# Kernel tuning notes

Measured on AMD Instinct MI355X. Metric: run time of the kernel, lower is better.

Reference implementation:

```python
import jax, jax.numpy as jnp
import numpy as np

K_UPPER = 196608  # number of smallest-|grad| positions to mask per sample


def setup_inputs() -> dict:
    key = jax.random.key(0)
    k1, k2 = jax.random.split(key)
    x = jax.random.normal(k1, (64, 3, 512, 512), dtype=jnp.float32)
    grad = jax.random.normal(k2, (64, 3, 512, 512), dtype=jnp.float32)
    return {"x": x, "grad": grad}


def _mask_low_gradient(x, grad):
    # x, grad: [B, C, H, W]
    B, C, H, W = x.shape
    hw = H * W
    flat_g = grad.reshape(B, -1)                                  # [B, C*H*W]
    # _sort: k smallest absolute gradients -> top_k of negated abs (unsorted ok)
    _neg_vals, idx = jax.lax.top_k(-jnp.abs(flat_g), K_UPPER)     # idx: [B, K]
    # channel containing each selected flat index (matches the torch range test)
    ch = idx // hw                                                # [B, K]
    xc = x.reshape(B, C, hw)
    # Faithful to source: torch slice [start:channel_indexes] EXCLUDES the last
    # element of each channel when computing min/max.
    mn = jnp.min(xc[:, :, : hw - 1], axis=-1)                     # [B, C]
    mx = jnp.max(xc[:, :, : hw - 1], axis=-1)                     # [B, C]
    lo = jnp.take_along_axis(mn, ch, axis=1)                      # [B, K]
    hi = jnp.take_along_axis(mx, ch, axis=1)                      # [B, K]
    # uniform fill in [lo, hi) per masked element
    u = jax.random.uniform(jax.random.key(42), idx.shape, dtype=x.dtype)
    fill = lo + u * (hi - lo)                                     # [B, K]
    flat_x = x.reshape(B, -1)
    out = flat_x.at[jnp.arange(B)[:, None], idx].set(fill)
    return out.reshape(x.shape)


def reference(x, grad):
    return _mask_low_gradient(x, grad)
```

## Files before the change

kernel.cpp:

```cpp
#include <hip/hip_runtime.h>
#include <stdint.h>

#define TPB 256
#define TPS 1024

constexpr int BN   = 64;
constexpr int CCH  = 3;
constexpr int HWS  = 262144;
constexpr int LOG_HW = 18;
constexpr int NPS  = 786432;
constexpr int KSEL = 196608;
constexpr int KCAP = 200704;
constexpr int NB_T = 32;
constexpr int CH_T = NPS / NB_T;
constexpr int NB_C = 64;
constexpr int CH_C = NPS / NB_C;
constexpr int WCH  = CH_C / 4;
constexpr int NB_S = 8;
constexpr int CH_S = KCAP / NB_S;
constexpr int TILE = 4096;
constexpr int NBINS = 2048;
constexpr int SUB  = 8;

constexpr int WS_MN   = 0;
constexpr int WS_MX   = 192;
constexpr int WS_V1   = 384;
constexpr int WS_B1   = 448;
constexpr int WS_GS   = 512;
constexpr int WS_KP   = 576;
constexpr int WS_S0   = 640;
constexpr int WS_S01  = 704;
constexpr int WS_CNT  = 768;
constexpr int WS_COFF = WS_CNT + BN * 256;
constexpr int WS_MNP  = WS_COFF + BN * 256;
constexpr int WS_MXP  = WS_MNP + BN * CCH * SUB;
constexpr int WS_CHC  = WS_MXP + BN * CCH * SUB;
constexpr int WS_THA  = WS_CHC + BN * 4;
constexpr int WS_THB  = WS_THA + BN * NBINS;
constexpr int WS_H0   = WS_THB + BN * NBINS;
constexpr int WS_H1   = WS_H0 + BN * 256 * NB_S;
constexpr int WS_H2   = WS_H1 + BN * 256 * NB_S;
constexpr int WS_H3   = WS_H2 + BN * 256 * NB_S;
constexpr size_t WS_FIX_END = (size_t)WS_H3 + (size_t)BN * 256 * NB_S;
constexpr size_t RECW = (size_t)BN * KCAP * 2;
constexpr size_t WS_NEEDED_BYTES = (WS_FIX_END + 2 * RECW) * 4;

__device__ __forceinline__ unsigned rotl32(unsigned x, int r) { return (x << r) | (x >> (32 - r)); }

__device__ __forceinline__ void tf4(unsigned& x0, unsigned& x1, int a, int b, int c, int d) {
  x0 += x1; x1 = rotl32(x1, a); x1 ^= x0;
  x0 += x1; x1 = rotl32(x1, b); x1 ^= x0;
  x0 += x1; x1 = rotl32(x1, c); x1 ^= x0;
  x0 += x1; x1 = rotl32(x1, d); x1 ^= x0;
}

__device__ __forceinline__ void threefry2x32(unsigned k0, unsigned k1, unsigned c0, unsigned c1,
                                             unsigned& o0, unsigned& o1) {
  const unsigned ks2 = k0 ^ k1 ^ 0x1BD11BDAu;
  unsigned x0 = c0 + k0, x1 = c1 + k1;
  tf4(x0, x1, 13, 15, 26, 6);  x0 += k1;  x1 += ks2 + 1u;
  tf4(x0, x1, 17, 29, 16, 24); x0 += ks2; x1 += k0 + 2u;
  tf4(x0, x1, 13, 15, 26, 6);  x0 += k0;  x1 += k1 + 3u;
  tf4(x0, x1, 17, 29, 16, 24); x0 += k1;  x1 += ks2 + 4u;
  tf4(x0, x1, 13, 15, 26, 6);  x0 += ks2; x1 += k0 + 5u;
  o0 = x0; o1 = x1;
}

__global__ __launch_bounds__(TPB) void k_zero(unsigned* __restrict__ p, int n) {
  int i = blockIdx.x * TPB + threadIdx.x;
  if (i < n) p[i] = 0u;
}

__global__ __launch_bounds__(TPB) void k_mnmx(const float4* __restrict__ x,
                                              unsigned* __restrict__ ws) {
  __shared__ float smn[TPB], smx[TPB];
  const int g = blockIdx.x;
  const int bc = g / SUB, sub = g - bc * SUB;
  const int Q4 = HWS / 4 / SUB;
  const size_t base4 = (size_t)bc * (HWS / 4) + (size_t)sub * Q4;
  const bool last = (sub == SUB - 1);
  const int tid = threadIdx.x;
  float lo = 3.4e38f, hi = -3.4e38f;
  for (int i = tid; i < Q4; i += TPB) {
    float4 v = x[base4 + i];
    if (last && i == Q4 - 1) {
      lo = fminf(lo, fminf(fminf(v.x, v.y), v.z));
      hi = fmaxf(hi, fmaxf(fmaxf(v.x, v.y), v.z));
    } else {
      lo = fminf(lo, fminf(fminf(v.x, v.y), fminf(v.z, v.w)));
      hi = fmaxf(hi, fmaxf(fmaxf(v.x, v.y), fmaxf(v.z, v.w)));
    }
  }
  smn[tid] = lo; smx[tid] = hi; __syncthreads();
  for (int s = TPB / 2; s > 0; s >>= 1) {
    if (tid < s) { smn[tid] = fminf(smn[tid], smn[tid + s]); smx[tid] = fmaxf(smx[tid], smx[tid + s]); }
    __syncthreads();
  }
  if (tid == 0) {
    ((float*)(ws + WS_MNP))[g] = smn[0];
    ((float*)(ws + WS_MXP))[g] = smx[0];
  }
}

__global__ __launch_bounds__(TPB) void k_mnfin(unsigned* __restrict__ ws) {
  const int t = threadIdx.x;
  if (t < BN * CCH) {
    const float* mnp = (const float*)(ws + WS_MNP);
    const float* mxp = (const float*)(ws + WS_MXP);
    float lo = 3.4e38f, hi = -3.4e38f;
    for (int s = 0; s < SUB; ++s) {
      lo = fminf(lo, mnp[t * SUB + s]);
      hi = fmaxf(hi, mxp[t * SUB + s]);
    }
    ((float*)(ws + WS_MN))[t] = lo;
    ((float*)(ws + WS_MX))[t] = hi;
  }
}

__global__ __launch_bounds__(TPB) void k_thrA(const unsigned* __restrict__ gb, unsigned* __restrict__ hist) {
  __shared__ unsigned h[NBINS];
  const int b = blockIdx.y, blk = blockIdx.x, tid = threadIdx.x;
  for (int v = tid; v < NBINS; v += TPB) h[v] = 0u;
  __syncthreads();
  const uint4* g4 = (const uint4*)(gb + (size_t)b * NPS + (size_t)blk * CH_T);
  for (int i = tid; i < CH_T / 4; i += TPB) {
    uint4 v = g4[i];
    atomicAdd(&h[(v.x & 0x7FFFFFFFu) >> 21], 1u);
    atomicAdd(&h[(v.y & 0x7FFFFFFFu) >> 21], 1u);
    atomicAdd(&h[(v.z & 0x7FFFFFFFu) >> 21], 1u);
    atomicAdd(&h[(v.w & 0x7FFFFFFFu) >> 21], 1u);
  }
  __syncthreads();
  unsigned* gh = hist + (size_t)b * NBINS;
  for (int v = tid; v < NBINS; v += TPB) if (h[v]) atomicAdd(&gh[v], h[v]);
}

__global__ __launch_bounds__(TPB) void k_thrB(const unsigned* __restrict__ gb,
                                              unsigned* __restrict__ hist,
                                              const unsigned* __restrict__ ws) {
  __shared__ unsigned h[NBINS];
  const int b = blockIdx.y, blk = blockIdx.x, tid = threadIdx.x;
  for (int v = tid; v < NBINS; v += TPB) h[v] = 0u;
  __syncthreads();
  const unsigned sel = ws[WS_V1 + b];
  const uint4* g4 = (const uint4*)(gb + (size_t)b * NPS + (size_t)blk * CH_T);
  for (int i = tid; i < CH_T / 4; i += TPB) {
    uint4 v = g4[i];
    unsigned a0 = v.x & 0x7FFFFFFFu, a1 = v.y & 0x7FFFFFFFu;
    unsigned a2 = v.z & 0x7FFFFFFFu, a3 = v.w & 0x7FFFFFFFu;
    if ((a0 >> 21) == sel) atomicAdd(&h[(a0 >> 10) & 2047u], 1u);
    if ((a1 >> 21) == sel) atomicAdd(&h[(a1 >> 10) & 2047u], 1u);
    if ((a2 >> 21) == sel) atomicAdd(&h[(a2 >> 10) & 2047u], 1u);
    if ((a3 >> 21) == sel) atomicAdd(&h[(a3 >> 10) & 2047u], 1u);
  }
  __syncthreads();
  unsigned* gh = hist + (size_t)b * NBINS;
  for (int v = tid; v < NBINS; v += TPB) if (h[v]) atomicAdd(&gh[v], h[v]);
}

__global__ __launch_bounds__(TPB) void k_find(const unsigned* __restrict__ hist,
                                              unsigned* __restrict__ ws, int mode) {
  __shared__ unsigned part[TPB];
  const int b = blockIdx.x, tid = threadIdx.x;
  const unsigned* h = hist + (size_t)b * NBINS;
  const int per = NBINS / TPB;
  const unsigned Kt = (mode == 0) ? (unsigned)KSEL : (unsigned)KSEL - ws[WS_B1 + b];
  unsigned vals[8];
  unsigned s = 0;
  for (int j = 0; j < per; ++j) { vals[j] = h[tid * per + j]; s += vals[j]; }
  part[tid] = s; __syncthreads();
  for (int off = 1; off < TPB; off <<= 1) {
    unsigned t = (tid >= off) ? part[tid - off] : 0u;
    __syncthreads(); part[tid] += t; __syncthreads();
  }
  unsigned run = part[tid] - s;
  for (int j = 0; j < per; ++j) {
    const unsigned lo = run, c = vals[j];
    run += c;
    if (lo < Kt && Kt <= run) {
      const unsigned v = (unsigned)(tid * per + j);
      if (mode == 0) {
        ws[WS_V1 + b] = v; ws[WS_B1 + b] = lo;
      } else {
        const unsigned T22 = (ws[WS_V1 + b] << 11) | v;
        ws[WS_GS + b] = (T22 << 10) | 1023u;
        unsigned kp = ws[WS_B1 + b] + lo + c;
        if (kp > (unsigned)KCAP) kp = (unsigned)KCAP;
        ws[WS_KP + b] = kp;
      }
    }
  }
}

__global__ __launch_bounds__(TPB) void k_ccount(const unsigned* __restrict__ gb, unsigned* __restrict__ ws) {
  __shared__ unsigned chs[3];
  const int b = blockIdx.y, blk = blockIdx.x, tid = threadIdx.x;
  const int lane = tid & 63, wv = tid >> 6;
  if (tid < 3) chs[tid] = 0u;
  __syncthreads();
  const unsigned G = ws[WS_GS + b];
  const uint4* g4 = (const uint4*)(gb + (size_t)b * NPS + (size_t)blk * CH_C) + wv * (WCH / 4);
  const unsigned e0 = (unsigned)blk * CH_C + (unsigned)wv * WCH;
  unsigned cnt = 0, cc0 = 0, cc1 = 0, cc2 = 0;
  for (int it = 0; it < WCH / 256; ++it) {
    const uint4 v = g4[it * 64 + lane];
    const unsigned e = e0 + (unsigned)it * 256u + (unsigned)lane * 4u;
    const unsigned k[4] = { v.x & 0x7FFFFFFFu, v.y & 0x7FFFFFFFu, v.z & 0x7FFFFFFFu, v.w & 0x7FFFFFFFu };
#pragma unroll
    for (int c = 0; c < 4; ++c) {
      if (k[c] <= G) {
        ++cnt;
        const unsigned ch = (e + (unsigned)c) >> LOG_HW;
        if (ch == 0) ++cc0; else if (ch == 1) ++cc1; else ++cc2;
      }
    }
  }
  for (int off = 32; off >= 1; off >>= 1) cnt += __shfl_down(cnt, off, 64);
  if (lane == 0) ws[WS_CNT + b * 256 + blk * 4 + wv] = cnt;
  if (cc0) atomicAdd(&chs[0], cc0);
  if (cc1) atomicAdd(&chs[1], cc1);
  if (cc2) atomicAdd(&chs[2], cc2);
  __syncthreads();
  if (tid < 3 && chs[tid]) atomicAdd(&ws[WS_CHC + b * 4 + tid], chs[tid]);
}

__global__ __launch_bounds__(TPB) void k_cscan(unsigned* __restrict__ ws) {
  __shared__ unsigned wsum[4];
  const int b = blockIdx.x, tid = threadIdx.x;
  const int lane = tid & 63, wv = tid >> 6;
  const unsigned cnt = ws[WS_CNT + b * 256 + tid];
  unsigned incl = cnt;
  for (int off = 1; off < 64; off <<= 1) {
    unsigned t = __shfl_up(incl, off, 64);
    if (lane >= off) incl += t;
  }
  if (lane == 63) wsum[wv] = incl;
  __syncthreads();
  unsigned wpre = 0;
  for (int w = 0; w < wv; ++w) wpre += wsum[w];
  ws[WS_COFF + b * 256 + tid] = incl - cnt + wpre;
  if (tid == 0) {
    const unsigned s0 = ws[WS_CHC + b * 4 + 0];
    ws[WS_S0 + b] = s0;
    ws[WS_S01 + b] = s0 + ws[WS_CHC + b * 4 + 1];
  }
}

__global__ __launch_bounds__(TPB) void k_cscatter(const unsigned* __restrict__ gb,
                                                  const unsigned* __restrict__ ws,
                                                  unsigned* __restrict__ keyArr,
                                                  unsigned* __restrict__ H0) {
  __shared__ unsigned h2[256 * NB_S];
  const int b = blockIdx.y, blk = blockIdx.x, tid = threadIdx.x;
  const int lane = tid & 63, wv = tid >> 6;
  for (int e = tid; e < 256 * NB_S; e += TPB) h2[e] = 0u;
  __syncthreads();
  const unsigned G = ws[WS_GS + b];
  unsigned base = ws[WS_COFF + b * 256 + blk * 4 + wv];
  const uint4* g4 = (const uint4*)(gb + (size_t)b * NPS + (size_t)blk * CH_C) + wv * (WCH / 4);
  unsigned* ka = keyArr + (size_t)b * KCAP;
  for (int it = 0; it < WCH / 256; ++it) {
    const uint4 v = g4[it * 64 + lane];
    unsigned k[4] = { v.x & 0x7FFFFFFFu, v.y & 0x7FFFFFFFu, v.z & 0x7FFFFFFFu, v.w & 0x7FFFFFFFu };
    bool s[4];
    unsigned cnt = 0;
#pragma unroll
    for (int c = 0; c < 4; ++c) { s[c] = (k[c] <= G); cnt += (unsigned)s[c]; }
    unsigned incl = cnt;
    for (int off = 1; off < 64; off <<= 1) {
      unsigned u = __shfl_up(incl, off, 64);
      if (lane >= off) incl += u;
    }
    const unsigned wtot = __shfl(incl, 63, 64);
    unsigned pos = base + incl - cnt;
#pragma unroll
    for (int c = 0; c < 4; ++c) {
      if (s[c]) {
        if (pos < (unsigned)KCAP) {
          ka[pos] = k[c];
          atomicAdd(&h2[(k[c] & 255u) * NB_S + pos / (unsigned)CH_S], 1u);
        }
        ++pos;
      }
    }
    base += wtot;
  }
  __syncthreads();
  unsigned* Hb = H0 + (size_t)b * 256 * NB_S;
  for (int e = tid; e < 256 * NB_S; e += TPB) {
    unsigned c = h2[e];
    if (c) atomicAdd(&Hb[e], c);
  }
}

__global__ __launch_bounds__(TPB) void k_hscan(unsigned* __restrict__ H) {
  __shared__ unsigned wsum[4];
  const int b = blockIdx.x, tid = threadIdx.x;
  const int lane = tid & 63, wv = tid >> 6;
  unsigned* Hb = H + (size_t)b * 256 * NB_S;
  unsigned row[NB_S];
  unsigned run = 0;
#pragma unroll
  for (int k = 0; k < NB_S; ++k) {
    unsigned t = Hb[tid * NB_S + k];
    row[k] = run; run += t;
  }
  unsigned incl = run;
  for (int off = 1; off < 64; off <<= 1) {
    unsigned t = __shfl_up(incl, off, 64);
    if (lane >= off) incl += t;
  }
  if (lane == 63) wsum[wv] = incl;
  __syncthreads();
  unsigned wpre = 0;
  for (int w = 0; w < wv; ++w) wpre += wsum[w];
  const unsigned excl = incl - run + wpre;
#pragma unroll
  for (int k = 0; k < NB_S; ++k) Hb[tid * NB_S + k] = row[k] + excl;
}

template<int MODE>
__global__ __launch_bounds__(TPS) void k_sort8(const unsigned* __restrict__ keyIn,
                                               const uint2* __restrict__ inR,
                                               uint2* __restrict__ outR,
                                               unsigned* __restrict__ fillmap,
                                               const unsigned* __restrict__ Hcur,
                                               unsigned* __restrict__ Hnext,
                                               const unsigned* __restrict__ ws,
                                               int shift) {
  __shared__ unsigned wh[16][256];
  __shared__ unsigned gout[256];
  __shared__ unsigned gbase[256];
  __shared__ unsigned wsum[4];
  __shared__ uint2    stg[(MODE == 2) ? 1 : TILE];
  __shared__ unsigned h2[(MODE == 2) ? 1 : 256 * NB_S];
  const int b = blockIdx.y, blk = blockIdx.x, tid = threadIdx.x;
  const int lane = tid & 63, wv = tid >> 6;
  const unsigned long long ltm = (1ull << lane) - 1ull;
  const unsigned kp = min(ws[WS_KP + b], (unsigned)KCAP);
  const unsigned s0 = (unsigned)blk * CH_S;
  const unsigned s1 = min(s0 + (unsigned)CH_S, kp);
  const unsigned* ki = keyIn + (size_t)b * KCAP;
  const uint2* in = inR + (size_t)b * KCAP;
  uint2* out = outR + (size_t)b * KCAP;
  unsigned* fm = fillmap + (size_t)b * KCAP;

  unsigned S0 = 0, S01 = 0;
  float l0 = 0, l1 = 0, l2 = 0, h0 = 0, h1 = 0, h2v = 0;
  if (MODE == 2) {
    S0 = ws[WS_S0 + b]; S01 = ws[WS_S01 + b];
    const float* mnf = (const float*)(ws + WS_MN);
    const float* mxf = (const float*)(ws + WS_MX);
    l0 = mnf[b * CCH]; l1 = mnf[b * CCH + 1]; l2 = mnf[b * CCH + 2];
    h0 = mxf[b * CCH]; h1 = mxf[b * CCH + 1]; h2v = mxf[b * CCH + 2];
  }

  for (int d = tid; d < 256; d += TPS) gbase[d] = Hcur[((size_t)b * 256 + d) * NB_S + blk];
  if (MODE != 2) for (int e = tid; e < 256 * NB_S; e += TPS) h2[e] = 0u;
  __syncthreads();

  for (unsigned t0 = s0; t0 < s1; t0 += (unsigned)TILE) {
    { uint4* w4 = (uint4*)&wh[0][0];
      w4[tid] = make_uint4(0u, 0u, 0u, 0u); }
    __syncthreads();

    unsigned key[4], cpp[4], wloc[4], dig[4];
    bool val[4];
    const unsigned wbase = t0 + (unsigned)wv * 256u;
#pragma unroll
    for (int c = 0; c < 4; ++c) {
      const unsigned i = wbase + (unsigned)c * 64u + (unsigned)lane;
      val[c] = (i < s1);
      if (MODE == 0) { cpp[c] = i; key[c] = val[c] ? ki[i] : 0u; }
      else { uint2 r = val[c] ? in[i] : make_uint2(0u, 0u); cpp[c] = r.x; key[c] = r.y; }
      dig[c] = (key[c] >> shift) & 255u;
      unsigned long long peers = __ballot(val[c]);
#pragma unroll
      for (int bit = 0; bit < 8; ++bit) {
        unsigned long long bb = __ballot(val[c] && ((dig[c] >> bit) & 1u));
        peers &= ((dig[c] >> bit) & 1u) ? bb : ~bb;
      }
      const unsigned before = (unsigned)__popcll(peers & ltm);
      int ldr = __ffsll((unsigned long long)peers) - 1;
      if (ldr < 0) ldr = 0;
      unsigned old = 0;
      if (val[c] && lane == ldr) old = atomicAdd(&wh[wv][dig[c]], (unsigned)__popcll(peers));
      old = __shfl(old, ldr, 64);
      wloc[c] = old + before;
    }
    __syncthreads();

    unsigned incl = 0, tot = 0;
    if (tid < 256) {
      const unsigned d = (unsigned)tid;
#pragma unroll
      for (int w = 0; w < 16; ++w) tot += wh[w][d];
      incl = tot;
      for (int off = 1; off < 64; off <<= 1) {
        unsigned t = __shfl_up(incl, off, 64);
        if (lane >= off) incl += t;
      }
      if (lane == 63) wsum[wv] = incl;
    }
    __syncthreads();
    if (tid < 256) {
      const unsigned d = (unsigned)tid;
      unsigned wpre = 0;
      for (int w = 0; w < wv; ++w) wpre += wsum[w];
      const unsigned tstart = incl - tot + wpre;
      const unsigned g = gbase[d];
      gout[d] = g - tstart;
      gbase[d] = g + tot;
      unsigned run = tstart;
#pragma unroll
      for (int w = 0; w < 16; ++w) { const unsigned t = wh[w][d]; wh[w][d] = run; run += t; }
    }
    __syncthreads();

    if (MODE != 2) {
#pragma unroll
      for (int c = 0; c < 4; ++c) {
        if (val[c]) {
          uint2 r; r.x = cpp[c]; r.y = key[c];
          stg[wh[wv][dig[c]] + wloc[c]] = r;
        }
      }
      __syncthreads();
      const unsigned nt = min((unsigned)TILE, s1 - t0);
      for (unsigned j = tid; j < nt; j += TPS) {
        const uint2 r = stg[j];
        const unsigned d = (r.y >> shift) & 255u;
        const unsigned pos = gout[d] + j;
        out[pos] = r;
        const unsigned nd = (r.y >> (shift + 8)) & 255u;
        atomicAdd(&h2[nd * NB_S + pos / (unsigned)CH_S], 1u);
      }
    } else {
#pragma unroll
      for (int c = 0; c < 4; ++c) {
        if (val[c]) {
          const unsigned rank = gout[dig[c]] + wh[wv][dig[c]] + wloc[c];
          unsigned res = 0xFFFFFFFFu;
          if (rank < (unsigned)KSEL) {
            const unsigned p = (unsigned)b * (unsigned)KSEL + rank;
            unsigned o0, o1;
            threefry2x32(0u, 42u, 0u, p, o0, o1);
            const unsigned bits = o0 ^ o1;
            const float u = __uint_as_float((bits >> 9) | 0x3f800000u) - 1.0f;
            const unsigned ch = (unsigned)(cpp[c] >= S0) + (unsigned)(cpp[c] >= S01);
            const float lo = (ch == 0) ? l0 : ((ch == 1) ? l1 : l2);
            const float hi = (ch == 0) ? h0 : ((ch == 1) ? h1 : h2v);
            res = __float_as_uint(lo + u * (hi - lo));
          }
          fm[cpp[c]] = res;
        }
      }
    }
    __syncthreads();
  }

  if (MODE != 2) {
    unsigned* Hb = Hnext + (size_t)b * 256 * NB_S;
    for (int e = tid; e < 256 * NB_S; e += TPS) {
      unsigned c = h2[e];
      if (c) atomicAdd(&Hb[e], c);
    }
  }
}

__global__ __launch_bounds__(TPB) void k_fill(const uint4* __restrict__ x4,
                                              const unsigned* __restrict__ gb,
                                              const unsigned* __restrict__ fillmap,
                                              const unsigned* __restrict__ ws,
                                              uint4* __restrict__ out4) {
  const int b = blockIdx.y, blk = blockIdx.x, tid = threadIdx.x;
  const int lane = tid & 63, wv = tid >> 6;
  const unsigned G = ws[WS_GS + b];
  const unsigned kp = min(ws[WS_KP + b], (unsigned)KCAP);
  unsigned base = ws[WS_COFF + b * 256 + blk * 4 + wv];
  const size_t t4 = (size_t)b * (NPS / 4) + (size_t)blk * (CH_C / 4) + (size_t)wv * (WCH / 4);
  const unsigned* fm = fillmap + (size_t)b * KCAP;
  for (int it = 0; it < WCH / 256; ++it) {
    const size_t a = t4 + it * 64 + lane;
    const uint4 gv = ((const uint4*)gb)[a];
    uint4 xv = x4[a];
    unsigned k[4] = { gv.x & 0x7FFFFFFFu, gv.y & 0x7FFFFFFFu, gv.z & 0x7FFFFFFFu, gv.w & 0x7FFFFFFFu };
    bool s[4];
    unsigned cnt = 0;
#pragma unroll
    for (int c = 0; c < 4; ++c) { s[c] = (k[c] <= G); cnt += (unsigned)s[c]; }
    unsigned incl = cnt;
    for (int off = 1; off < 64; off <<= 1) {
      unsigned u = __shfl_up(incl, off, 64);
      if (lane >= off) incl += u;
    }
    const unsigned wtot = __shfl(incl, 63, 64);
    unsigned pos = base + incl - cnt;
    unsigned* xw = (unsigned*)&xv;
#pragma unroll
    for (int c = 0; c < 4; ++c) {
      if (s[c]) {
        if (pos < kp) {
          const unsigned r = fm[pos];
          if (r != 0xFFFFFFFFu) xw[c] = r;
        }
        ++pos;
      }
    }
    out4[a] = xv;
    base += wtot;
  }
}

extern "C" void kernel_launch(void* const* d_in, const int* in_sizes, int n_in,
                              void* d_out, int out_size, void* d_ws, size_t ws_size,
                              hipStream_t stream) {
  const float* x = (const float*)d_in[0];
  const unsigned* gb = (const unsigned*)d_in[1];
  float* out = (float*)d_out;
  unsigned* ws = (unsigned*)d_ws;
  if (ws_size < WS_NEEDED_BYTES) return;

  unsigned* R1 = ws + WS_FIX_END;
  unsigned* R2 = ws + WS_FIX_END + RECW;
  unsigned* H0 = ws + WS_H0;
  unsigned* H1 = ws + WS_H1;
  unsigned* H2 = ws + WS_H2;
  unsigned* H3 = ws + WS_H3;

  dim3 blk(TPB);
  dim3 sblk(TPS);

  k_mnmx<<<dim3(BN * CCH * SUB), blk, 0, stream>>>((const float4*)x, ws);
  k_mnfin<<<dim3(1), blk, 0, stream>>>(ws);
  {
    const int nz = (int)(WS_FIX_END - WS_CHC);
    k_zero<<<dim3((nz + TPB - 1) / TPB), blk, 0, stream>>>(ws + WS_CHC, nz);
  }

  k_thrA<<<dim3(NB_T, BN), blk, 0, stream>>>(gb, ws + WS_THA);
  k_find<<<dim3(BN), blk, 0, stream>>>(ws + WS_THA, ws, 0);
  k_thrB<<<dim3(NB_T, BN), blk, 0, stream>>>(gb, ws + WS_THB, ws);
  k_find<<<dim3(BN), blk, 0, stream>>>(ws + WS_THB, ws, 1);

  k_ccount<<<dim3(NB_C, BN), blk, 0, stream>>>(gb, ws);
  k_cscan<<<dim3(BN), blk, 0, stream>>>(ws);
  k_cscatter<<<dim3(NB_C, BN), blk, 0, stream>>>(gb, ws, R1, H0);

  k_hscan<<<dim3(BN), blk, 0, stream>>>(H0);
  k_sort8<0><<<dim3(NB_S, BN), sblk, 0, stream>>>(R1, (const uint2*)nullptr, (uint2*)R2, nullptr, H0, H1, ws, 0);
  k_hscan<<<dim3(BN), blk, 0, stream>>>(H1);
  k_sort8<1><<<dim3(NB_S, BN), sblk, 0, stream>>>(nullptr, (const uint2*)R2, (uint2*)R1, nullptr, H1, H2, ws, 8);
  k_hscan<<<dim3(BN), blk, 0, stream>>>(H2);
  k_sort8<1><<<dim3(NB_S, BN), sblk, 0, stream>>>(nullptr, (const uint2*)R1, (uint2*)R2, nullptr, H2, H3, ws, 16);
  k_hscan<<<dim3(BN), blk, 0, stream>>>(H3);
  k_sort8<2><<<dim3(NB_S, BN), sblk, 0, stream>>>(nullptr, (const uint2*)R2, (uint2*)nullptr, R1, H3, nullptr, ws, 24);

  k_fill<<<dim3(NB_C, BN), blk, 0, stream>>>((const uint4*)x, gb, R1, ws, (uint4*)out);
}
```

Before: 779.5 us.

## Flatten grids batch-innermost, use 7-bit final digit, nontemporal loads/stores in fill

Changes several kernels from 2D grids to 1D grids in which the batch index varies fastest, which changes block scheduling order across the chip. The final radix pass now uses 7 digit bits instead of 8, since the top key bit is always cleared by the abs mask, which saves one ballot per element. The fill kernel switches to nontemporal vector loads and stores so the streaming data bypasses cache retention. Together these target scheduling locality, ballot work and cache pollution, with some risk that the new block order hurts locality.

```diff
diff --git a/kernel.cpp b/kernel.cpp
--- a/kernel.cpp
+++ b/kernel.cpp
@@ -21,6 +21,8 @@
 constexpr int TILE = 4096;
 constexpr int NBINS = 2048;
 constexpr int SUB  = 8;
+
+typedef unsigned u32x4 __attribute__((ext_vector_type(4)));
 
 constexpr int WS_MN   = 0;
 constexpr int WS_MX   = 192;
@@ -194,7 +196,8 @@
 
 __global__ __launch_bounds__(TPB) void k_ccount(const unsigned* __restrict__ gb, unsigned* __restrict__ ws) {
   __shared__ unsigned chs[3];
-  const int b = blockIdx.y, blk = blockIdx.x, tid = threadIdx.x;
+  const int bid = blockIdx.x;
+  const int b = bid & 63, blk = bid >> 6, tid = threadIdx.x;
   const int lane = tid & 63, wv = tid >> 6;
   if (tid < 3) chs[tid] = 0u;
   __syncthreads();
@@ -251,7 +254,8 @@
                                                   unsigned* __restrict__ keyArr,
                                                   unsigned* __restrict__ H0) {
   __shared__ unsigned h2[256 * NB_S];
-  const int b = blockIdx.y, blk = blockIdx.x, tid = threadIdx.x;
+  const int bid = blockIdx.x;
+  const int b = bid & 63, blk = bid >> 6, tid = threadIdx.x;
   const int lane = tid & 63, wv = tid >> 6;
   for (int e = tid; e < 256 * NB_S; e += TPB) h2[e] = 0u;
   __syncthreads();
@@ -328,13 +332,16 @@
                                                unsigned* __restrict__ Hnext,
                                                const unsigned* __restrict__ ws,
                                                int shift) {
+  constexpr int DBITS = (MODE == 2) ? 7 : 8;
+  constexpr unsigned DMASK = (1u << DBITS) - 1u;
   __shared__ unsigned wh[16][256];
   __shared__ unsigned gout[256];
   __shared__ unsigned gbase[256];
   __shared__ unsigned wsum[4];
   __shared__ uint2    stg[(MODE == 2) ? 1 : TILE];
   __shared__ unsigned h2[(MODE == 2) ? 1 : 256 * NB_S];
-  const int b = blockIdx.y, blk = blockIdx.x, tid = threadIdx.x;
+  const int bid = blockIdx.x;
+  const int b = bid & 63, blk = bid >> 6, tid = threadIdx.x;
   const int lane = tid & 63, wv = tid >> 6;
   const unsigned long long ltm = (1ull << lane) - 1ull;
   const unsigned kp = min(ws[WS_KP + b], (unsigned)KCAP);
@@ -373,10 +380,10 @@
       val[c] = (i < s1);
       if (MODE == 0) { cpp[c] = i; key[c] = val[c] ? ki[i] : 0u; }
       else { uint2 r = val[c] ? in[i] : make_uint2(0u, 0u); cpp[c] = r.x; key[c] = r.y; }
-      dig[c] = (key[c] >> shift) & 255u;
+      dig[c] = (key[c] >> shift) & DMASK;
       unsigned long long peers = __ballot(val[c]);
 #pragma unroll
-      for (int bit = 0; bit < 8; ++bit) {
+      for (int bit = 0; bit < DBITS; ++bit) {
         unsigned long long bb = __ballot(val[c] && ((dig[c] >> bit) & 1u));
         peers &= ((dig[c] >> bit) & 1u) ? bb : ~bb;
       }
@@ -468,12 +475,13 @@
   }
 }
 
-__global__ __launch_bounds__(TPB) void k_fill(const uint4* __restrict__ x4,
-                                              const unsigned* __restrict__ gb,
+__global__ __launch_bounds__(TPB) void k_fill(const u32x4* __restrict__ x4,
+                                              const u32x4* __restrict__ g4all,
                                               const unsigned* __restrict__ fillmap,
                                               const unsigned* __restrict__ ws,
-                                              uint4* __restrict__ out4) {
-  const int b = blockIdx.y, blk = blockIdx.x, tid = threadIdx.x;
+                                              u32x4* __restrict__ out4) {
+  const int bid = blockIdx.x;
+  const int b = bid & 63, blk = bid >> 6, tid = threadIdx.x;
   const int lane = tid & 63, wv = tid >> 6;
   const unsigned G = ws[WS_GS + b];
   const unsigned kp = min(ws[WS_KP + b], (unsigned)KCAP);
@@ -482,8 +490,8 @@
   const unsigned* fm = fillmap + (size_t)b * KCAP;
   for (int it = 0; it < WCH / 256; ++it) {
     const size_t a = t4 + it * 64 + lane;
-    const uint4 gv = ((const uint4*)gb)[a];
-    uint4 xv = x4[a];
+    const u32x4 gv = __builtin_nontemporal_load(&g4all[a]);
+    u32x4 xv = __builtin_nontemporal_load(&x4[a]);
     unsigned k[4] = { gv.x & 0x7FFFFFFFu, gv.y & 0x7FFFFFFFu, gv.z & 0x7FFFFFFFu, gv.w & 0x7FFFFFFFu };
     bool s[4];
     unsigned cnt = 0;
@@ -496,18 +504,17 @@
     }
     const unsigned wtot = __shfl(incl, 63, 64);
     unsigned pos = base + incl - cnt;
-    unsigned* xw = (unsigned*)&xv;
 #pragma unroll
     for (int c = 0; c < 4; ++c) {
       if (s[c]) {
         if (pos < kp) {
           const unsigned r = fm[pos];
-          if (r != 0xFFFFFFFFu) xw[c] = r;
+          if (r != 0xFFFFFFFFu) xv[c] = r;
         }
         ++pos;
       }
     }
-    out4[a] = xv;
+    __builtin_nontemporal_store(xv, &out4[a]);
     base += wtot;
   }
 }
@@ -543,18 +550,18 @@
   k_thrB<<<dim3(NB_T, BN), blk, 0, stream>>>(gb, ws + WS_THB, ws);
   k_find<<<dim3(BN), blk, 0, stream>>>(ws + WS_THB, ws, 1);
 
-  k_ccount<<<dim3(NB_C, BN), blk, 0, stream>>>(gb, ws);
+  k_ccount<<<dim3(NB_C * BN), blk, 0, stream>>>(gb, ws);
   k_cscan<<<dim3(BN), blk, 0, stream>>>(ws);
-  k_cscatter<<<dim3(NB_C, BN), blk, 0, stream>>>(gb, ws, R1, H0);
+  k_cscatter<<<dim3(NB_C * BN), blk, 0, stream>>>(gb, ws, R1, H0);
 
   k_hscan<<<dim3(BN), blk, 0, stream>>>(H0);
-  k_sort8<0><<<dim3(NB_S, BN), sblk, 0, stream>>>(R1, (const uint2*)nullptr, (uint2*)R2, nullptr, H0, H1, ws, 0);
+  k_sort8<0><<<dim3(NB_S * BN), sblk, 0, stream>>>(R1, (const uint2*)nullptr, (uint2*)R2, nullptr, H0, H1, ws, 0);
   k_hscan<<<dim3(BN), blk, 0, stream>>>(H1);
-  k_sort8<1><<<dim3(NB_S, BN), sblk, 0, stream>>>(nullptr, (const uint2*)R2, (uint2*)R1, nullptr, H1, H2, ws, 8);
+  k_sort8<1><<<dim3(NB_S * BN), sblk, 0, stream>>>(nullptr, (const uint2*)R2, (uint2*)R1, nullptr, H1, H2, ws, 8);
   k_hscan<<<dim3(BN), blk, 0, stream>>>(H2);
-  k_sort8<1><<<dim3(NB_S, BN), sblk, 0, stream>>>(nullptr, (const uint2*)R1, (uint2*)R2, nullptr, H2, H3, ws, 16);
+  k_sort8<1><<<dim3(NB_S * BN), sblk, 0, stream>>>(nullptr, (const uint2*)R1, (uint2*)R2, nullptr, H2, H3, ws, 16);
   k_hscan<<<dim3(BN), blk, 0, stream>>>(H3);
-  k_sort8<2><<<dim3(NB_S, BN), sblk, 0, stream>>>(nullptr, (const uint2*)R2, (uint2*)nullptr, R1, H3, nullptr, ws, 24);
-
-  k_fill<<<dim3(NB_C, BN), blk, 0, stream>>>((const uint4*)x, gb, R1, ws, (uint4*)out);
-}
+  k_sort8<2><<<dim3(NB_S * BN), sblk, 0, stream>>>(nullptr, (const uint2*)R2, (uint2*)nullptr, R1, H3, nullptr, ws, 24);
+
+  k_fill<<<dim3(NB_C * BN), blk, 0, stream>>>((const u32x4*)x, (const u32x4*)gb, R1, ws, (u32x4*)out);
+}
```

After: 768.6 us. Within noise of the previous version (-1.4%).
